# Optimization experiments

Hardware: AMD Instinct MI355X
Metric: run time of the kernel (lower is better)

Reference implementation:

```python
import jax, jax.numpy as jnp
import numpy as np

MATRIX_DIM = 128
FEAT = MATRIX_DIM * (MATRIX_DIM + 1) // 2  # 8256, triu incl. diagonal
HID = FEAT // 5                            # 1651
BATCH = 4096


def setup_inputs() -> dict:
    key = jax.random.key(0)
    k0, k1, k2, k3, k4 = jax.random.split(key, 5)
    stdv1 = 1.0 / FEAT / 2.0
    stdv2 = 1.0 / HID / 2.0
    return {
        "sim_matrices": jax.random.normal(k0, (BATCH, MATRIX_DIM, MATRIX_DIM), dtype=jnp.float32),
        "W1": jax.random.uniform(k1, (HID, FEAT), minval=-stdv1, maxval=stdv1, dtype=jnp.float32),
        "b1": jax.random.uniform(k2, (HID,), minval=-stdv1, maxval=stdv1, dtype=jnp.float32),
        "W2": jax.random.uniform(k3, (1, HID), minval=-stdv2, maxval=stdv2, dtype=jnp.float32),
        "b2": jax.random.uniform(k4, (1,), minval=-stdv2, maxval=stdv2, dtype=jnp.float32),
    }


def reference(sim_matrices, W1, b1, W2, b2):
    # flatten: take upper-triangular (incl. diag) entries -> [B, FEAT]
    iu0, iu1 = np.triu_indices(sim_matrices.shape[1])
    x = sim_matrices[:, iu0, iu1]
    # Linear_block 1 (ideal crossbar VMM = W x + b) + ReLU
    h = jax.nn.relu(jnp.einsum("bf,hf->bh", x, W1) + b1)
    # Linear_block 2 + Sigmoid -> [B, 1]
    return jax.nn.sigmoid(jnp.einsum("bh,oh->bo", h, W2) + b2)
```

## Files before the change

kernel.cpp:

```cpp
#include <hip/hip_runtime.h>
#include <hip/hip_bf16.h>
#include <math.h>

#define MDIM  128
#define FEAT  8256
#define HID   1651
#define HIDP  1664
#define BATCH 4096
#define BK    64
#define KT_TOTAL 129
#define NZ    2
#define KT_PER 64
#define W1SCALE 8192.0f
#define W1INV   (1.0f / 8192.0f)
#define DEPTH 3

using f32x4  = __attribute__((ext_vector_type(4))) float;
using f32x16 = __attribute__((ext_vector_type(16))) float;
using i32x4  = __attribute__((ext_vector_type(4))) int;
using i32x8  = __attribute__((ext_vector_type(8))) int;
using bf16x8 = __attribute__((ext_vector_type(8))) __bf16;
typedef long long i64;

__device__ __forceinline__ void gload_lds16(const void* g, void* l) {
    __builtin_amdgcn_global_load_lds(
        (const __attribute__((address_space(1))) void*)g,
        (__attribute__((address_space(3))) void*)l,
        16, 0, 0);
}

__device__ __forceinline__ int row_off(int i) { return (i * (257 - i)) >> 1; }

__device__ __forceinline__ void pack8_fp8(const float* f, int* o) {
    int lo = __builtin_amdgcn_cvt_pk_fp8_f32(f[0], f[1], 0, false);
    lo     = __builtin_amdgcn_cvt_pk_fp8_f32(f[2], f[3], lo, true);
    int hi = __builtin_amdgcn_cvt_pk_fp8_f32(f[4], f[5], 0, false);
    hi     = __builtin_amdgcn_cvt_pk_fp8_f32(f[6], f[7], hi, true);
    o[0] = lo; o[1] = hi;
}

__global__ void __launch_bounds__(256)
prep_kernel(const float* __restrict__ sim, const float* __restrict__ W1,
            char* __restrict__ X, char* __restrict__ W1p) {
    const int t = threadIdx.x;
    if (blockIdx.x < BATCH) {
        const int b = blockIdx.x;
        const float* srow = sim + ((i64)b << 14);
        char* dst = X + (i64)b * FEAT;
#pragma unroll
        for (int it = 0; it < 5; ++it) {
            const int w = it * 256 + t;
            if (w < FEAT / 8) {
                const int f0 = w * 8;
                int i = (int)((257.0f - sqrtf(66049.0f - 8.0f * (float)f0)) * 0.5f);
                i = i < 0 ? 0 : (i > 127 ? 127 : i);
                while (i < 127 && row_off(i + 1) <= f0) ++i;
                while (i > 0 && row_off(i) > f0) --i;
                int j = i + (f0 - row_off(i));
                float v[8];
#pragma unroll
                for (int e = 0; e < 8; ++e) {
                    if (j > 127) { ++i; j = i; }
                    v[e] = srow[i * MDIM + j];
                    ++j;
                }
                int o[2];
                pack8_fp8(v, o);
                *(int2*)(dst + f0) = make_int2(o[0], o[1]);
            }
        }
    } else {
        const int c  = blockIdx.x - BATCH;
        const int wb = c % 5;
        const int n  = c / 5;
        const int w  = wb * 256 + t;
        if (w >= FEAT / 8) return;
        const int f0 = w * 8;
        int o[2];
        if (n < HID) {
            const float* src = W1 + (i64)n * FEAT + f0;
            const f32x4 a = *(const f32x4*)src;
            const f32x4 d = *(const f32x4*)(src + 4);
            float v[8];
#pragma unroll
            for (int e = 0; e < 4; ++e) {
                v[e]     = a[e] * W1SCALE;
                v[e + 4] = d[e] * W1SCALE;
            }
            pack8_fp8(v, o);
        } else {
            o[0] = 0; o[1] = 0;
        }
        *(int2*)(W1p + (i64)n * FEAT + f0) = make_int2(o[0], o[1]);
    }
}

__global__ void __launch_bounds__(256, 3)
gemm_split_kernel(const char* __restrict__ X,
                  const char* __restrict__ W1p,
                  __hip_bfloat16* __restrict__ Cz) {
    __shared__ __align__(16) char lds_a[DEPTH * 8192];
    __shared__ __align__(16) char lds_b[DEPTH * 8192];

    const int t    = threadIdx.x;
    const int w    = t >> 6;
    const int l    = t & 63;
    const int bm   = blockIdx.x;
    const int bn   = blockIdx.y;
    const int z    = blockIdx.z;
    const int wm   = w >> 1;
    const int wn   = w & 1;
    const int lm   = l & 31;
    const int c0   = (l >> 5) << 1;

    f32x16 acc[2][2];
#pragma unroll
    for (int r = 0; r < 16; ++r) {
        acc[0][0][r] = 0.f; acc[0][1][r] = 0.f;
        acc[1][0][r] = 0.f; acc[1][1][r] = 0.f;
    }

    const int kt0 = z * KT_PER;
    const int nkt = (z == NZ - 1) ? (KT_TOTAL - KT_PER * (NZ - 1)) : KT_PER;

    const int stR = ((w & 1) << 6) + l;
    const char* gA0 = X + (i64)(bm * 128 + stR) * FEAT + kt0 * BK + (w >> 1) * 16;
    const char* gB0 = W1p + (i64)(bn * 128 + stR) * FEAT + kt0 * BK + (w >> 1) * 16;
    char* lA = lds_a + w * 1024;
    char* lB = lds_b + w * 1024;

#define STAGE(buf, kidx) do {                                      \
        const char* _ga = gA0 + (i64)(kidx) * BK;                  \
        const char* _gb = gB0 + (i64)(kidx) * BK;                  \
        char* _la = lA + (buf) * 8192;                             \
        char* _lb = lB + (buf) * 8192;                             \
        gload_lds16(_ga,      _la);                                \
        gload_lds16(_ga + 32, _la + 4096);                         \
        gload_lds16(_gb,      _lb);                                \
        gload_lds16(_gb + 32, _lb + 4096);                         \
    } while (0)

    STAGE(0, 0);
    STAGE(1, 1);
    STAGE(2, 2);

    int cur = 0;
    for (int kt = 0; kt < nkt; ++kt) {
        if (kt + 3 <= nkt)      asm volatile("s_waitcnt vmcnt(8)" ::: "memory");
        else if (kt + 2 == nkt) asm volatile("s_waitcnt vmcnt(4)" ::: "memory");
        else                    asm volatile("s_waitcnt vmcnt(0)" ::: "memory");
        __builtin_amdgcn_s_barrier();
        __builtin_amdgcn_sched_barrier(0);

        const char* pa = lds_a + cur * 8192 + c0 * 2048 + (wm * 64 + lm) * 16;
        const char* pb = lds_b + cur * 8192 + c0 * 2048 + (wn * 64 + lm) * 16;
        i32x8 A0, A1, B0, B1;
        *((i32x4*)&A0)     = *(const i32x4*)(pa);
        *((i32x4*)&A0 + 1) = *(const i32x4*)(pa + 2048);
        *((i32x4*)&A1)     = *(const i32x4*)(pa + 512);
        *((i32x4*)&A1 + 1) = *(const i32x4*)(pa + 512 + 2048);
        *((i32x4*)&B0)     = *(const i32x4*)(pb);
        *((i32x4*)&B0 + 1) = *(const i32x4*)(pb + 2048);
        *((i32x4*)&B1)     = *(const i32x4*)(pb + 512);
        *((i32x4*)&B1 + 1) = *(const i32x4*)(pb + 512 + 2048);

        __builtin_amdgcn_s_setprio(1);
        acc[0][0] = __builtin_amdgcn_mfma_scale_f32_32x32x64_f8f6f4(
            A0, B0, acc[0][0], 0, 0, 0, 0x7F7F7F7F, 0, 0x7F7F7F7F);
        acc[0][1] = __builtin_amdgcn_mfma_scale_f32_32x32x64_f8f6f4(
            A0, B1, acc[0][1], 0, 0, 0, 0x7F7F7F7F, 0, 0x7F7F7F7F);
        acc[1][0] = __builtin_amdgcn_mfma_scale_f32_32x32x64_f8f6f4(
            A1, B0, acc[1][0], 0, 0, 0, 0x7F7F7F7F, 0, 0x7F7F7F7F);
        acc[1][1] = __builtin_amdgcn_mfma_scale_f32_32x32x64_f8f6f4(
            A1, B1, acc[1][1], 0, 0, 0, 0x7F7F7F7F, 0, 0x7F7F7F7F);
        __builtin_amdgcn_s_setprio(0);

        asm volatile("s_waitcnt lgkmcnt(0)" ::: "memory");
        __builtin_amdgcn_sched_barrier(0);
        __builtin_amdgcn_s_barrier();
        __builtin_amdgcn_sched_barrier(0);

        if (kt + 3 < nkt) STAGE(cur, kt + 3);
        cur = (cur == DEPTH - 1) ? 0 : cur + 1;
    }
#undef STAGE

    __hip_bfloat16* cz = Cz + ((i64)z * BATCH + bm * 128) * HIDP
                            + bn * 128 + wn * 64;
#pragma unroll
    for (int rb = 0; rb < 2; ++rb)
#pragma unroll
        for (int cb = 0; cb < 2; ++cb) {
#pragma unroll
            for (int reg = 0; reg < 16; ++reg) {
                const int row = (reg & 3) + ((reg >> 2) << 3) + ((l >> 5) << 2);
                const int ml  = wm * 64 + rb * 32 + row;
                cz[(i64)ml * HIDP + cb * 32 + lm] =
                    __float2bfloat16(acc[rb][cb][reg]);
            }
        }
}

__global__ void __launch_bounds__(256)
epilogue_kernel(const __hip_bfloat16* __restrict__ Cz,
                const float* __restrict__ b1,
                const float* __restrict__ W2,
                const float* __restrict__ b2,
                float* __restrict__ out) {
    const int b = blockIdx.x;
    const int t = threadIdx.x;
    float sum = 0.0f;
    const bf16x8* r0 = (const bf16x8*)(Cz + (i64)b * HIDP);
    const bf16x8* r1 = (const bf16x8*)(Cz + ((i64)BATCH + b) * HIDP);
    if (t < HIDP / 8) {
        const bf16x8 a = r0[t];
        const bf16x8 c = r1[t];
#pragma unroll
        for (int e = 0; e < 8; ++e) {
            const int n = t * 8 + e;
            if (n < HID) {
                const float v = ((float)a[e] + (float)c[e]) * W1INV + b1[n];
                sum += fmaxf(v, 0.0f) * W2[n];
            }
        }
    }
    sum += __shfl_xor(sum, 1);
    sum += __shfl_xor(sum, 2);
    sum += __shfl_xor(sum, 4);
    sum += __shfl_xor(sum, 8);
    sum += __shfl_xor(sum, 16);
    sum += __shfl_xor(sum, 32);
    __shared__ float wsum[4];
    if ((t & 63) == 0) wsum[t >> 6] = sum;
    __syncthreads();
    if (t == 0) {
        const float s = wsum[0] + wsum[1] + wsum[2] + wsum[3];
        out[b] = 1.0f / (1.0f + expf(-(s + b2[0])));
    }
}

extern "C" void kernel_launch(void* const* d_in, const int* in_sizes, int n_in,
                              void* d_out, int out_size, void* d_ws, size_t ws_size,
                              hipStream_t stream) {
    const float* sim = (const float*)d_in[0];
    const float* W1  = (const float*)d_in[1];
    const float* b1  = (const float*)d_in[2];
    const float* W2  = (const float*)d_in[3];
    const float* b2  = (const float*)d_in[4];
    float* out = (float*)d_out;

    char* ws = (char*)d_ws;
    const i64 X_OFF   = 0;
    const i64 W1P_OFF = (i64)BATCH * FEAT;
    const i64 CZ_OFF  = W1P_OFF + (i64)HIDP * FEAT;
    char*           Xf8  = ws + X_OFF;
    char*           W1f8 = ws + W1P_OFF;
    __hip_bfloat16* Cz   = (__hip_bfloat16*)(ws + CZ_OFF);

    prep_kernel<<<BATCH + 5 * HIDP, 256, 0, stream>>>(sim, W1, Xf8, W1f8);
    {
        dim3 grid(BATCH / 128, HIDP / 128, NZ);
        gemm_split_kernel<<<grid, 256, 0, stream>>>(Xf8, W1f8, Cz);
    }
    epilogue_kernel<<<BATCH, 256, 0, stream>>>(Cz, b1, W2, b2, out);
}
```

Before: 527.4 us.

## Fuse layer-2 epilogue into GEMM with atomics and drop split-K

Removes the split-K partial output buffer and separate epilogue kernel; the GEMM now applies bias, ReLU and the W2 dot product in registers, reduces across lanes, and atomically accumulates per-row sums, followed by a tiny sigmoid kernel. The prep kernel gains an extra block to zero the accumulation buffer. This avoids writing and rereading the bf16 intermediate, at the cost of halving the number of GEMM blocks (each doing the full K loop) and adding float atomics with nondeterministic summation order.

```diff
diff --git a/kernel.cpp b/kernel.cpp
--- a/kernel.cpp
+++ b/kernel.cpp
@@ -9,8 +9,6 @@
 #define BATCH 4096
 #define BK    64
 #define KT_TOTAL 129
-#define NZ    2
-#define KT_PER 64
 #define W1SCALE 8192.0f
 #define W1INV   (1.0f / 8192.0f)
 #define DEPTH 3
@@ -19,7 +17,6 @@
 using f32x16 = __attribute__((ext_vector_type(16))) float;
 using i32x4  = __attribute__((ext_vector_type(4))) int;
 using i32x8  = __attribute__((ext_vector_type(8))) int;
-using bf16x8 = __attribute__((ext_vector_type(8))) __bf16;
 typedef long long i64;
 
 __device__ __forceinline__ void gload_lds16(const void* g, void* l) {
@@ -41,7 +38,8 @@
 
 __global__ void __launch_bounds__(256)
 prep_kernel(const float* __restrict__ sim, const float* __restrict__ W1,
-            char* __restrict__ X, char* __restrict__ W1p) {
+            char* __restrict__ X, char* __restrict__ W1p,
+            float* __restrict__ out_pre) {
     const int t = threadIdx.x;
     if (blockIdx.x < BATCH) {
         const int b = blockIdx.x;
@@ -69,7 +67,7 @@
                 *(int2*)(dst + f0) = make_int2(o[0], o[1]);
             }
         }
-    } else {
+    } else if (blockIdx.x < BATCH + 5 * HIDP) {
         const int c  = blockIdx.x - BATCH;
         const int wb = c % 5;
         const int n  = c / 5;
@@ -92,13 +90,19 @@
             o[0] = 0; o[1] = 0;
         }
         *(int2*)(W1p + (i64)n * FEAT + f0) = make_int2(o[0], o[1]);
+    } else {
+        const f32x4 zz = {0.f, 0.f, 0.f, 0.f};
+        f32x4* p = (f32x4*)out_pre + t * 4;
+        p[0] = zz; p[1] = zz; p[2] = zz; p[3] = zz;
     }
 }
 
 __global__ void __launch_bounds__(256, 3)
-gemm_split_kernel(const char* __restrict__ X,
+gemm_fused_kernel(const char* __restrict__ X,
                   const char* __restrict__ W1p,
-                  __hip_bfloat16* __restrict__ Cz) {
+                  const float* __restrict__ b1,
+                  const float* __restrict__ W2,
+                  float* __restrict__ out_pre) {
     __shared__ __align__(16) char lds_a[DEPTH * 8192];
     __shared__ __align__(16) char lds_b[DEPTH * 8192];
 
@@ -107,7 +111,6 @@
     const int l    = t & 63;
     const int bm   = blockIdx.x;
     const int bn   = blockIdx.y;
-    const int z    = blockIdx.z;
     const int wm   = w >> 1;
     const int wn   = w & 1;
     const int lm   = l & 31;
@@ -120,12 +123,11 @@
         acc[1][0][r] = 0.f; acc[1][1][r] = 0.f;
     }
 
-    const int kt0 = z * KT_PER;
-    const int nkt = (z == NZ - 1) ? (KT_TOTAL - KT_PER * (NZ - 1)) : KT_PER;
+    const int nkt = KT_TOTAL;
 
     const int stR = ((w & 1) << 6) + l;
-    const char* gA0 = X + (i64)(bm * 128 + stR) * FEAT + kt0 * BK + (w >> 1) * 16;
-    const char* gB0 = W1p + (i64)(bn * 128 + stR) * FEAT + kt0 * BK + (w >> 1) * 16;
+    const char* gA0 = X + (i64)(bm * 128 + stR) * FEAT + (w >> 1) * 16;
+    const char* gB0 = W1p + (i64)(bn * 128 + stR) * FEAT + (w >> 1) * 16;
     char* lA = lds_a + w * 1024;
     char* lB = lds_b + w * 1024;
 
@@ -185,58 +187,44 @@
     }
 #undef STAGE
 
-    __hip_bfloat16* cz = Cz + ((i64)z * BATCH + bm * 128) * HIDP
-                            + bn * 128 + wn * 64;
+    const int colbase = bn * 128 + wn * 64 + lm;
+    float b1v[2], w2v[2];
+#pragma unroll
+    for (int cb = 0; cb < 2; ++cb) {
+        const int col = colbase + cb * 32;
+        const bool ok = col < HID;
+        b1v[cb] = ok ? b1[col] : 0.f;
+        w2v[cb] = ok ? W2[col] : 0.f;
+    }
+    const int rbase = bm * 128 + wm * 64 + ((l >> 5) << 2);
 #pragma unroll
     for (int rb = 0; rb < 2; ++rb)
 #pragma unroll
-        for (int cb = 0; cb < 2; ++cb) {
-#pragma unroll
-            for (int reg = 0; reg < 16; ++reg) {
-                const int row = (reg & 3) + ((reg >> 2) << 3) + ((l >> 5) << 2);
-                const int ml  = wm * 64 + rb * 32 + row;
-                cz[(i64)ml * HIDP + cb * 32 + lm] =
-                    __float2bfloat16(acc[rb][cb][reg]);
+        for (int reg = 0; reg < 16; ++reg) {
+            float v = 0.f;
+#pragma unroll
+            for (int cb = 0; cb < 2; ++cb) {
+                const float pre = acc[rb][cb][reg] * W1INV + b1v[cb];
+                v += fmaxf(pre, 0.f) * w2v[cb];
+            }
+            v += __shfl_xor(v, 1);
+            v += __shfl_xor(v, 2);
+            v += __shfl_xor(v, 4);
+            v += __shfl_xor(v, 8);
+            v += __shfl_xor(v, 16);
+            if (lm == 0) {
+                const int row = rbase + rb * 32 + (reg & 3) + ((reg >> 2) << 3);
+                atomicAdd(out_pre + row, v);
             }
         }
 }
 
 __global__ void __launch_bounds__(256)
-epilogue_kernel(const __hip_bfloat16* __restrict__ Cz,
-                const float* __restrict__ b1,
-                const float* __restrict__ W2,
-                const float* __restrict__ b2,
-                float* __restrict__ out) {
-    const int b = blockIdx.x;
-    const int t = threadIdx.x;
-    float sum = 0.0f;
-    const bf16x8* r0 = (const bf16x8*)(Cz + (i64)b * HIDP);
-    const bf16x8* r1 = (const bf16x8*)(Cz + ((i64)BATCH + b) * HIDP);
-    if (t < HIDP / 8) {
-        const bf16x8 a = r0[t];
-        const bf16x8 c = r1[t];
-#pragma unroll
-        for (int e = 0; e < 8; ++e) {
-            const int n = t * 8 + e;
-            if (n < HID) {
-                const float v = ((float)a[e] + (float)c[e]) * W1INV + b1[n];
-                sum += fmaxf(v, 0.0f) * W2[n];
-            }
-        }
-    }
-    sum += __shfl_xor(sum, 1);
-    sum += __shfl_xor(sum, 2);
-    sum += __shfl_xor(sum, 4);
-    sum += __shfl_xor(sum, 8);
-    sum += __shfl_xor(sum, 16);
-    sum += __shfl_xor(sum, 32);
-    __shared__ float wsum[4];
-    if ((t & 63) == 0) wsum[t >> 6] = sum;
-    __syncthreads();
-    if (t == 0) {
-        const float s = wsum[0] + wsum[1] + wsum[2] + wsum[3];
-        out[b] = 1.0f / (1.0f + expf(-(s + b2[0])));
-    }
+sigmoid_kernel(const float* __restrict__ pre,
+               const float* __restrict__ b2,
+               float* __restrict__ out) {
+    const int i = blockIdx.x * 256 + threadIdx.x;
+    out[i] = 1.0f / (1.0f + expf(-(pre[i] + b2[0])));
 }
 
 extern "C" void kernel_launch(void* const* d_in, const int* in_sizes, int n_in,
@@ -252,15 +240,15 @@
     char* ws = (char*)d_ws;
     const i64 X_OFF   = 0;
     const i64 W1P_OFF = (i64)BATCH * FEAT;
-    const i64 CZ_OFF  = W1P_OFF + (i64)HIDP * FEAT;
-    char*           Xf8  = ws + X_OFF;
-    char*           W1f8 = ws + W1P_OFF;
-    __hip_bfloat16* Cz   = (__hip_bfloat16*)(ws + CZ_OFF);
-
-    prep_kernel<<<BATCH + 5 * HIDP, 256, 0, stream>>>(sim, W1, Xf8, W1f8);
+    const i64 PRE_OFF = W1P_OFF + (i64)HIDP * FEAT;
+    char*  Xf8  = ws + X_OFF;
+    char*  W1f8 = ws + W1P_OFF;
+    float* pre  = (float*)(ws + PRE_OFF);
+
+    prep_kernel<<<BATCH + 5 * HIDP + 1, 256, 0, stream>>>(sim, W1, Xf8, W1f8, pre);
     {
-        dim3 grid(BATCH / 128, HIDP / 128, NZ);
-        gemm_split_kernel<<<grid, 256, 0, stream>>>(Xf8, W1f8, Cz);
-    }
-    epilogue_kernel<<<BATCH, 256, 0, stream>>>(Cz, b1, W2, b2, out);
-}
+        dim3 grid(BATCH / 128, HIDP / 128);
+        gemm_fused_kernel<<<grid, 256, 0, stream>>>(Xf8, W1f8, b1, W2, pre);
+    }
+    sigmoid_kernel<<<BATCH / 256, 256, 0, stream>>>(pre, b2, out);
+}
```

Measured after the change: 501.9 us. 4.8% less time.
